# Kernel tuning notes

Hardware: AMD Instinct MI355X
Metric: run time of the kernel (lower is better)

Reference implementation:

```python
import jax, jax.numpy as jnp
import numpy as np

B, NNODES = 65536, 32
D_IN, D_G, D_C, H, D_OUT = 16, 8, 16, 64, 4


def setup_inputs() -> dict:
    key = jax.random.key(0)
    ks = jax.random.split(key, 24)
    N = B * NNODES
    x = jax.random.normal(ks[0], (N, D_IN), jnp.float32)
    other_obs = jax.random.normal(ks[1], (B, D_C), jnp.float32)
    # star graph per batch element with reverse edges: (0->j) and (j->0)
    bs = np.concatenate([np.zeros(NNODES - 1, np.int32), np.arange(1, NNODES, dtype=np.int32)])
    bd = np.concatenate([np.arange(1, NNODES, dtype=np.int32), np.zeros(NNODES - 1, np.int32)])
    offs = (np.arange(B, dtype=np.int32) * NNODES)[:, None]
    src = jnp.asarray((bs[None, :] + offs).reshape(-1))
    dst = jnp.asarray((bd[None, :] + offs).reshape(-1))
    node_seg = jnp.asarray(np.repeat(np.arange(B, dtype=np.int32), NNODES))
    s = 0.1
    p = lambda k, sh: jax.random.normal(k, sh, jnp.float32) * s
    return dict(
        x=x, other_obs=other_obs, src=src, dst=dst, node_seg=node_seg,
        Wp1=p(ks[2], (D_IN, D_G)), bp1=jnp.zeros((D_G,), jnp.float32),
        Ws1=p(ks[3], (D_IN, D_G)), Wn1=p(ks[4], (D_G, D_G)), bc1=jnp.zeros((D_G,), jnp.float32),
        Wp2=p(ks[5], (D_G, D_G)), bp2=jnp.zeros((D_G,), jnp.float32),
        Ws2=p(ks[6], (D_G, D_G)), Wn2=p(ks[7], (D_G, D_G)), bc2=jnp.zeros((D_G,), jnp.float32),
        W1=p(ks[8], (D_C + D_G, H)), bf1=jnp.zeros((H,), jnp.float32),
        W2=p(ks[9], (H, H)), bf2=jnp.zeros((H,), jnp.float32),
        W3=p(ks[10], (H, H)), bf3=jnp.zeros((H,), jnp.float32),
        W4=jax.random.uniform(ks[11], (H, D_OUT), jnp.float32, -0.003, 0.003),
        bf4=jnp.zeros((D_OUT,), jnp.float32),
    )


def _sage_pool(h, src, dst, Wp, bp, Ws, Wn, bc, num_nodes):
    # DGL SAGEConv aggregator_type='pool': relu(fc_pool(h_src)), scatter-max to dst
    m = jax.nn.relu(h @ Wp + bp)[src]              # [E, D_G]
    agg = jax.ops.segment_max(m, dst, num_segments=num_nodes)
    agg = jnp.where(jnp.isfinite(agg), agg, 0.0)   # empty-neighbor nodes -> 0 (DGL default)
    return h @ Ws + agg @ Wn + bc


def reference(x, other_obs, src, dst, node_seg,
              Wp1, bp1, Ws1, Wn1, bc1,
              Wp2, bp2, Ws2, Wn2, bc2,
              W1, bf1, W2, bf2, W3, bf3, W4, bf4):
    N = x.shape[0]
    Bn = other_obs.shape[0]
    n_per = N // Bn
    h = jnp.tanh(_sage_pool(x, src, dst, Wp1, bp1, Ws1, Wn1, bc1, N))  # conv1 activation=tanh
    h = _sage_pool(h, src, dst, Wp2, bp2, Ws2, Wn2, bc2, N)            # conv2, no activation
    pooled = jax.ops.segment_sum(h, node_seg, num_segments=Bn) / n_per  # AvgPooling (fixed n)
    res = jnp.concatenate([pooled, other_obs], axis=1)
    h1 = jax.nn.relu(res @ W1 + bf1)
    h2 = jax.nn.relu(h1 @ W2 + bf2)
    h3 = jax.nn.relu(h2 @ W3 + bf3)
    return jnp.tanh(h3 @ W4 + bf4)
```

## Files before the change

### kernel.cpp

```cpp
#include <hip/hip_runtime.h>


typedef float v2f __attribute__((ext_vector_type(2)));
__device__ __forceinline__ v2f fma2(v2f a, v2f b, v2f c) {
  return __builtin_elementwise_fma(a, b, c);
}
__device__ __forceinline__ v2f ld2(const float* p) { return *(const v2f*)p; }

__device__ __forceinline__ float fast_tanh(float v) {
  v = fminf(fmaxf(v, -10.f), 10.f);
  float e = exp2f(v * 2.8853900817779268f);
  return 1.f - 2.f * __builtin_amdgcn_rcpf(e + 1.f);
}

template<int CTRL, int RMASK>
__device__ __forceinline__ float dpp0(float v) {
  return __int_as_float(__builtin_amdgcn_update_dpp(
      0, __float_as_int(v), CTRL, RMASK, 0xf, true));
}
__device__ __forceinline__ float red_max32(float t) {
  t = fmaxf(t, dpp0<0x111, 0xf>(t));
  t = fmaxf(t, dpp0<0x112, 0xf>(t));
  t = fmaxf(t, dpp0<0x114, 0xf>(t));
  t = fmaxf(t, dpp0<0x118, 0xf>(t));
  t = fmaxf(t, dpp0<0x142, 0xa>(t));
  return t;
}
__device__ __forceinline__ float red_sum32(float t) {
  t += dpp0<0x111, 0xf>(t);
  t += dpp0<0x112, 0xf>(t);
  t += dpp0<0x114, 0xf>(t);
  t += dpp0<0x118, 0xf>(t);
  t += dpp0<0x142, 0xa>(t);
  return t;
}
__device__ __forceinline__ float bcast31(float v) {
  return __int_as_float(__builtin_amdgcn_ds_swizzle(__float_as_int(v), 0x03E0));
}

__global__ __launch_bounds__(256, 4) void conv_kernel(
    const float* __restrict__ x,
    const float* __restrict__ Wp1, const float* __restrict__ bp1,
    const float* __restrict__ Ws1, const float* __restrict__ Wn1,
    const float* __restrict__ bc1,
    const float* __restrict__ Wp2, const float* __restrict__ bp2,
    float* __restrict__ res) {
  const int lane = threadIdx.x & 63;
  const int pair = blockIdx.x * 4 + (threadIdx.x >> 6);
  const int nl = lane & 31, s = lane >> 5;
  const int node = 31 - nl;
  const int b = pair * 2 + s;
  const bool isn0 = (nl == 31);

  const float4* xp = (const float4*)(x + ((size_t)b * 32 + node) * 16);
  float4 a0 = xp[0], a1 = xp[1], a2 = xp[2], a3 = xp[3];
  float xr[16] = {a0.x,a0.y,a0.z,a0.w, a1.x,a1.y,a1.z,a1.w,
                  a2.x,a2.y,a2.z,a2.w, a3.x,a3.y,a3.z,a3.w};

  v2f mv[4], sv[4];
  #pragma unroll
  for (int i = 0; i < 4; i++) { mv[i] = ld2(bp1 + 2*i); sv[i] = ld2(bc1 + 2*i); }
  #pragma unroll
  for (int f = 0; f < 16; f++) {
    v2f xv = {xr[f], xr[f]};
    #pragma unroll
    for (int i = 0; i < 4; i++) {
      mv[i] = fma2(xv, ld2(Wp1 + f*8 + 2*i), mv[i]);
      sv[i] = fma2(xv, ld2(Ws1 + f*8 + 2*i), sv[i]);
    }
  }
  float m[8];
  #pragma unroll
  for (int i = 0; i < 4; i++) {
    m[2*i]   = fmaxf(mv[i].x, 0.f);
    m[2*i+1] = fmaxf(mv[i].y, 0.f);
  }

  float agg[8];
  #pragma unroll
  for (int g = 0; g < 8; g++) {
    float t = isn0 ? 0.f : m[g];
    t = red_max32(t);
    float b0v = bcast31(m[g]);
    agg[g] = isn0 ? t : b0v;
  }
  #pragma unroll
  for (int j = 0; j < 8; j++) {
    v2f av = {agg[j], agg[j]};
    #pragma unroll
    for (int i = 0; i < 4; i++) sv[i] = fma2(av, ld2(Wn1 + j*8 + 2*i), sv[i]);
  }
  float h[8];
  #pragma unroll
  for (int i = 0; i < 4; i++) {
    h[2*i]   = fast_tanh(sv[i].x);
    h[2*i+1] = fast_tanh(sv[i].y);
  }

  v2f m2v[4];
  #pragma unroll
  for (int i = 0; i < 4; i++) m2v[i] = ld2(bp2 + 2*i);
  #pragma unroll
  for (int j = 0; j < 8; j++) {
    v2f hv = {h[j], h[j]};
    #pragma unroll
    for (int i = 0; i < 4; i++) m2v[i] = fma2(hv, ld2(Wp2 + j*8 + 2*i), m2v[i]);
  }
  float m2[8];
  #pragma unroll
  for (int i = 0; i < 4; i++) {
    m2[2*i]   = fmaxf(m2v[i].x, 0.f);
    m2[2*i+1] = fmaxf(m2v[i].y, 0.f);
  }

  float outv[16];
  #pragma unroll
  for (int g = 0; g < 8; g++) outv[g] = red_sum32(h[g]);
  #pragma unroll
  for (int g = 0; g < 8; g++) {
    float t = isn0 ? 0.f : m2[g];
    t = red_max32(t);
    outv[8+g] = fmaf(31.f, m2[g], t);
  }
  if (isn0) {
    float4* rp = (float4*)(res + (size_t)b * 16);
    rp[0] = make_float4(outv[0],  outv[1],  outv[2],  outv[3]);
    rp[1] = make_float4(outv[4],  outv[5],  outv[6],  outv[7]);
    rp[2] = make_float4(outv[8],  outv[9],  outv[10], outv[11]);
    rp[3] = make_float4(outv[12], outv[13], outv[14], outv[15]);
  }
}

#define HSTR 65
__global__ __launch_bounds__(256, 3) void mlp_kernel(
    const float* __restrict__ res, const float* __restrict__ obs,
    const float* __restrict__ Ws2, const float* __restrict__ Wn2,
    const float* __restrict__ bc2,
    const float* __restrict__ W1, const float* __restrict__ bf1,
    const float* __restrict__ W2, const float* __restrict__ bf2,
    const float* __restrict__ W3, const float* __restrict__ bf3,
    const float* __restrict__ W4, const float* __restrict__ bf4,
    float* __restrict__ out) {
  __shared__ float hx[64 * HSTR];
  const int tid  = threadIdx.x;
  const int lane = tid & 63;
  const int p    = __builtin_amdgcn_readfirstlane(tid >> 6);
  const int b    = blockIdx.x * 64 + lane;
  const int ob0  = p * 16;

  const float4* rp = (const float4*)(res + (size_t)b * 16);
  float4 r0 = rp[0], r1 = rp[1], r2 = rp[2], r3 = rp[3];
  const float4* op = (const float4*)(obs + (size_t)b * 16);
  float4 o0 = op[0], o1 = op[1], o2 = op[2], o3 = op[3];
  float rm[8] = {r0.x,r0.y,r0.z,r0.w, r1.x,r1.y,r1.z,r1.w};
  float ag[8] = {r2.x,r2.y,r2.z,r2.w, r3.x,r3.y,r3.z,r3.w};
  float ob[16] = {o0.x,o0.y,o0.z,o0.w, o1.x,o1.y,o1.z,o1.w,
                  o2.x,o2.y,o2.z,o2.w, o3.x,o3.y,o3.z,o3.w};

  v2f pv[4];
  #pragma unroll
  for (int i = 0; i < 4; i++) pv[i] = (v2f){0.f, 0.f};
  #pragma unroll
  for (int j = 0; j < 8; j++) {
    v2f rv = {rm[j], rm[j]}, av = {ag[j], ag[j]};
    #pragma unroll
    for (int i = 0; i < 4; i++) {
      pv[i] = fma2(rv, ld2(Ws2 + j*8 + 2*i), pv[i]);
      pv[i] = fma2(av, ld2(Wn2 + j*8 + 2*i), pv[i]);
    }
  }
  float pooled[8];
  #pragma unroll
  for (int i = 0; i < 4; i++) {
    pooled[2*i]   = fmaf(pv[i].x, 1.f/32.f, bc2[2*i]);
    pooled[2*i+1] = fmaf(pv[i].y, 1.f/32.f, bc2[2*i+1]);
  }

  v2f acc[8];
  #pragma unroll
  for (int i = 0; i < 8; i++) acc[i] = ld2(bf1 + ob0 + 2*i);
  #pragma unroll
  for (int j = 0; j < 8; j++) {
    v2f sj = {pooled[j], pooled[j]};
    #pragma unroll
    for (int i = 0; i < 8; i++) acc[i] = fma2(sj, ld2(W1 + j*64 + ob0 + 2*i), acc[i]);
  }
  #pragma unroll
  for (int j = 0; j < 16; j++) {
    v2f sj = {ob[j], ob[j]};
    #pragma unroll
    for (int i = 0; i < 8; i++) acc[i] = fma2(sj, ld2(W1 + (8+j)*64 + ob0 + 2*i), acc[i]);
  }
  #pragma unroll
  for (int i = 0; i < 8; i++) {
    hx[lane*HSTR + ob0 + 2*i]   = fmaxf(acc[i].x, 0.f);
    hx[lane*HSTR + ob0 + 2*i+1] = fmaxf(acc[i].y, 0.f);
  }
  __syncthreads();
  float h[64];
  #pragma unroll
  for (int k = 0; k < 64; k++) h[k] = hx[lane*HSTR + k];
  __syncthreads();

  #pragma unroll
  for (int i = 0; i < 8; i++) acc[i] = ld2(bf2 + ob0 + 2*i);
  #pragma unroll
  for (int k = 0; k < 64; k++) {
    v2f hk = {h[k], h[k]};
    #pragma unroll
    for (int i = 0; i < 8; i++) acc[i] = fma2(hk, ld2(W2 + k*64 + ob0 + 2*i), acc[i]);
  }
  #pragma unroll
  for (int i = 0; i < 8; i++) {
    hx[lane*HSTR + ob0 + 2*i]   = fmaxf(acc[i].x, 0.f);
    hx[lane*HSTR + ob0 + 2*i+1] = fmaxf(acc[i].y, 0.f);
  }
  __syncthreads();
  #pragma unroll
  for (int k = 0; k < 64; k++) h[k] = hx[lane*HSTR + k];
  __syncthreads();

  #pragma unroll
  for (int i = 0; i < 8; i++) acc[i] = ld2(bf3 + ob0 + 2*i);
  #pragma unroll
  for (int k = 0; k < 64; k++) {
    v2f hk = {h[k], h[k]};
    #pragma unroll
    for (int i = 0; i < 8; i++) acc[i] = fma2(hk, ld2(W3 + k*64 + ob0 + 2*i), acc[i]);
  }
  #pragma unroll
  for (int i = 0; i < 8; i++) {
    hx[lane*HSTR + ob0 + 2*i]   = fmaxf(acc[i].x, 0.f);
    hx[lane*HSTR + ob0 + 2*i+1] = fmaxf(acc[i].y, 0.f);
  }
  __syncthreads();

  if (p == 0) {
    #pragma unroll
    for (int k = 0; k < 64; k++) h[k] = hx[lane*HSTR + k];
    v2f o4a = ld2(bf4), o4b = ld2(bf4 + 2);
    #pragma unroll
    for (int k = 0; k < 64; k++) {
      v2f hk = {h[k], h[k]};
      o4a = fma2(hk, ld2(W4 + k*4),     o4a);
      o4b = fma2(hk, ld2(W4 + k*4 + 2), o4b);
    }
    ((float4*)out)[b] = make_float4(fast_tanh(o4a.x), fast_tanh(o4a.y),
                                    fast_tanh(o4b.x), fast_tanh(o4b.y));
  }
}

extern "C" void kernel_launch(void* const* d_in, const int* in_sizes, int n_in,
                              void* d_out, int out_size, void* d_ws, size_t ws_size,
                              hipStream_t stream) {
  const float* x   = (const float*)d_in[0];
  const float* obs = (const float*)d_in[1];
  const float* Wp1 = (const float*)d_in[5];
  const float* bp1 = (const float*)d_in[6];
  const float* Ws1 = (const float*)d_in[7];
  const float* Wn1 = (const float*)d_in[8];
  const float* bc1 = (const float*)d_in[9];
  const float* Wp2 = (const float*)d_in[10];
  const float* bp2 = (const float*)d_in[11];
  const float* Ws2 = (const float*)d_in[12];
  const float* Wn2 = (const float*)d_in[13];
  const float* bc2 = (const float*)d_in[14];
  const float* W1  = (const float*)d_in[15];
  const float* bf1 = (const float*)d_in[16];
  const float* W2  = (const float*)d_in[17];
  const float* bf2 = (const float*)d_in[18];
  const float* W3  = (const float*)d_in[19];
  const float* bf3 = (const float*)d_in[20];
  const float* W4  = (const float*)d_in[21];
  const float* bf4 = (const float*)d_in[22];
  float* res = (float*)d_ws;
  float* out = (float*)d_out;

  hipLaunchKernelGGL(conv_kernel, dim3(8192), dim3(256), 0, stream,
                     x, Wp1, bp1, Ws1, Wn1, bc1, Wp2, bp2, res);
  hipLaunchKernelGGL(mlp_kernel, dim3(1024), dim3(256), 0, stream,
                     res, obs, Ws2, Wn2, bc2, W1, bf1, W2, bf2, W3, bf3, W4, bf4, out);
}
```

Measured before the change: 283.0 us.

## Process two nodes per lane in conv kernel with 16-lane graph groups

Each lane now handles two nodes of a batch graph, so a graph occupies 16 lanes instead of 32 and the grid is halved. Cross-lane max and sum reductions drop one DPP step, and the two nodes are combined inside the lane before reducing. Weight loads are shared between the two nodes, which cuts reduction and broadcast overhead per node. In exchange each thread holds more registers, which may lower occupancy, and each lane reads 32 contiguous floats per node pair.

New measurement: 285.8 us. About the same (+1.0%).

```diff
diff --git a/kernel.cpp b/kernel.cpp
--- a/kernel.cpp
+++ b/kernel.cpp
@@ -18,24 +18,46 @@
   return __int_as_float(__builtin_amdgcn_update_dpp(
       0, __float_as_int(v), CTRL, RMASK, 0xf, true));
 }
-__device__ __forceinline__ float red_max32(float t) {
+__device__ __forceinline__ float red_max16(float t) {
   t = fmaxf(t, dpp0<0x111, 0xf>(t));
   t = fmaxf(t, dpp0<0x112, 0xf>(t));
   t = fmaxf(t, dpp0<0x114, 0xf>(t));
   t = fmaxf(t, dpp0<0x118, 0xf>(t));
-  t = fmaxf(t, dpp0<0x142, 0xa>(t));
   return t;
 }
-__device__ __forceinline__ float red_sum32(float t) {
+__device__ __forceinline__ float red_sum16(float t) {
   t += dpp0<0x111, 0xf>(t);
   t += dpp0<0x112, 0xf>(t);
   t += dpp0<0x114, 0xf>(t);
   t += dpp0<0x118, 0xf>(t);
-  t += dpp0<0x142, 0xa>(t);
   return t;
 }
-__device__ __forceinline__ float bcast31(float v) {
-  return __int_as_float(__builtin_amdgcn_ds_swizzle(__float_as_int(v), 0x03E0));
+__device__ __forceinline__ float bcast15(float v) {
+  return __int_as_float(__builtin_amdgcn_ds_swizzle(__float_as_int(v), 0x01F0));
+}
+
+__device__ __forceinline__ void conv1_node(
+    const float xr[16],
+    const float* __restrict__ Wp1, const float* __restrict__ bp1,
+    const float* __restrict__ Ws1, const float* __restrict__ bc1,
+    float m[8], v2f sv[4]) {
+  v2f mv[4];
+  #pragma unroll
+  for (int i = 0; i < 4; i++) { mv[i] = ld2(bp1 + 2*i); sv[i] = ld2(bc1 + 2*i); }
+  #pragma unroll
+  for (int f = 0; f < 16; f++) {
+    v2f xv = {xr[f], xr[f]};
+    #pragma unroll
+    for (int i = 0; i < 4; i++) {
+      mv[i] = fma2(xv, ld2(Wp1 + f*8 + 2*i), mv[i]);
+      sv[i] = fma2(xv, ld2(Ws1 + f*8 + 2*i), sv[i]);
+    }
+  }
+  #pragma unroll
+  for (int i = 0; i < 4; i++) {
+    m[2*i]   = fmaxf(mv[i].x, 0.f);
+    m[2*i+1] = fmaxf(mv[i].y, 0.f);
+  }
 }
 
 __global__ __launch_bounds__(256, 4) void conv_kernel(
@@ -45,82 +67,89 @@
     const float* __restrict__ bc1,
     const float* __restrict__ Wp2, const float* __restrict__ bp2,
     float* __restrict__ res) {
-  const int lane = threadIdx.x & 63;
-  const int pair = blockIdx.x * 4 + (threadIdx.x >> 6);
-  const int nl = lane & 31, s = lane >> 5;
-  const int node = 31 - nl;
-  const int b = pair * 2 + s;
-  const bool isn0 = (nl == 31);
-
-  const float4* xp = (const float4*)(x + ((size_t)b * 32 + node) * 16);
-  float4 a0 = xp[0], a1 = xp[1], a2 = xp[2], a3 = xp[3];
-  float xr[16] = {a0.x,a0.y,a0.z,a0.w, a1.x,a1.y,a1.z,a1.w,
-                  a2.x,a2.y,a2.z,a2.w, a3.x,a3.y,a3.z,a3.w};
-
-  v2f mv[4], sv[4];
-  #pragma unroll
-  for (int i = 0; i < 4; i++) { mv[i] = ld2(bp1 + 2*i); sv[i] = ld2(bc1 + 2*i); }
-  #pragma unroll
-  for (int f = 0; f < 16; f++) {
-    v2f xv = {xr[f], xr[f]};
+  const int tid  = threadIdx.x;
+  const int lane = tid & 63;
+  const int l    = lane & 15;
+  const int row  = lane >> 4;
+  const int b    = blockIdx.x * 16 + (tid >> 6) * 4 + row;
+  const int nA   = 30 - 2*l;
+  const bool isn0 = (l == 15);
+
+  const float4* xp = (const float4*)(x + ((size_t)b * 32 + nA) * 16);
+
+  float mA[8], mB[8];
+  v2f svA[4], svB[4];
+  {
+    float4 a0 = xp[0], a1 = xp[1], a2 = xp[2], a3 = xp[3];
+    float xr[16] = {a0.x,a0.y,a0.z,a0.w, a1.x,a1.y,a1.z,a1.w,
+                    a2.x,a2.y,a2.z,a2.w, a3.x,a3.y,a3.z,a3.w};
+    conv1_node(xr, Wp1, bp1, Ws1, bc1, mA, svA);
+  }
+  {
+    float4 a0 = xp[4], a1 = xp[5], a2 = xp[6], a3 = xp[7];
+    float xr[16] = {a0.x,a0.y,a0.z,a0.w, a1.x,a1.y,a1.z,a1.w,
+                    a2.x,a2.y,a2.z,a2.w, a3.x,a3.y,a3.z,a3.w};
+    conv1_node(xr, Wp1, bp1, Ws1, bc1, mB, svB);
+  }
+
+  float aggA[8], aggB[8];
+  #pragma unroll
+  for (int g = 0; g < 8; g++) {
+    float t = isn0 ? mB[g] : fmaxf(mA[g], mB[g]);
+    t = red_max16(t);
+    float b0v = bcast15(mA[g]);
+    aggA[g] = isn0 ? t : b0v;
+    aggB[g] = b0v;
+  }
+  #pragma unroll
+  for (int j = 0; j < 8; j++) {
+    v2f avA = {aggA[j], aggA[j]}, avB = {aggB[j], aggB[j]};
     #pragma unroll
     for (int i = 0; i < 4; i++) {
-      mv[i] = fma2(xv, ld2(Wp1 + f*8 + 2*i), mv[i]);
-      sv[i] = fma2(xv, ld2(Ws1 + f*8 + 2*i), sv[i]);
-    }
-  }
-  float m[8];
+      v2f w = ld2(Wn1 + j*8 + 2*i);
+      svA[i] = fma2(avA, w, svA[i]);
+      svB[i] = fma2(avB, w, svB[i]);
+    }
+  }
+  float hA[8], hB[8];
   #pragma unroll
   for (int i = 0; i < 4; i++) {
-    m[2*i]   = fmaxf(mv[i].x, 0.f);
-    m[2*i+1] = fmaxf(mv[i].y, 0.f);
-  }
-
-  float agg[8];
+    hA[2*i]   = fast_tanh(svA[i].x);
+    hA[2*i+1] = fast_tanh(svA[i].y);
+    hB[2*i]   = fast_tanh(svB[i].x);
+    hB[2*i+1] = fast_tanh(svB[i].y);
+  }
+
+  v2f m2vA[4], m2vB[4];
+  #pragma unroll
+  for (int i = 0; i < 4; i++) { m2vA[i] = ld2(bp2 + 2*i); m2vB[i] = m2vA[i]; }
+  #pragma unroll
+  for (int j = 0; j < 8; j++) {
+    v2f hvA = {hA[j], hA[j]}, hvB = {hB[j], hB[j]};
+    #pragma unroll
+    for (int i = 0; i < 4; i++) {
+      v2f w = ld2(Wp2 + j*8 + 2*i);
+      m2vA[i] = fma2(hvA, w, m2vA[i]);
+      m2vB[i] = fma2(hvB, w, m2vB[i]);
+    }
+  }
+  float m2A[8], m2B[8];
+  #pragma unroll
+  for (int i = 0; i < 4; i++) {
+    m2A[2*i]   = fmaxf(m2vA[i].x, 0.f);
+    m2A[2*i+1] = fmaxf(m2vA[i].y, 0.f);
+    m2B[2*i]   = fmaxf(m2vB[i].x, 0.f);
+    m2B[2*i+1] = fmaxf(m2vB[i].y, 0.f);
+  }
+
+  float outv[16];
+  #pragma unroll
+  for (int g = 0; g < 8; g++) outv[g] = red_sum16(hA[g] + hB[g]);
   #pragma unroll
   for (int g = 0; g < 8; g++) {
-    float t = isn0 ? 0.f : m[g];
-    t = red_max32(t);
-    float b0v = bcast31(m[g]);
-    agg[g] = isn0 ? t : b0v;
-  }
-  #pragma unroll
-  for (int j = 0; j < 8; j++) {
-    v2f av = {agg[j], agg[j]};
-    #pragma unroll
-    for (int i = 0; i < 4; i++) sv[i] = fma2(av, ld2(Wn1 + j*8 + 2*i), sv[i]);
-  }
-  float h[8];
-  #pragma unroll
-  for (int i = 0; i < 4; i++) {
-    h[2*i]   = fast_tanh(sv[i].x);
-    h[2*i+1] = fast_tanh(sv[i].y);
-  }
-
-  v2f m2v[4];
-  #pragma unroll
-  for (int i = 0; i < 4; i++) m2v[i] = ld2(bp2 + 2*i);
-  #pragma unroll
-  for (int j = 0; j < 8; j++) {
-    v2f hv = {h[j], h[j]};
-    #pragma unroll
-    for (int i = 0; i < 4; i++) m2v[i] = fma2(hv, ld2(Wp2 + j*8 + 2*i), m2v[i]);
-  }
-  float m2[8];
-  #pragma unroll
-  for (int i = 0; i < 4; i++) {
-    m2[2*i]   = fmaxf(m2v[i].x, 0.f);
-    m2[2*i+1] = fmaxf(m2v[i].y, 0.f);
-  }
-
-  float outv[16];
-  #pragma unroll
-  for (int g = 0; g < 8; g++) outv[g] = red_sum32(h[g]);
-  #pragma unroll
-  for (int g = 0; g < 8; g++) {
-    float t = isn0 ? 0.f : m2[g];
-    t = red_max32(t);
-    outv[8+g] = fmaf(31.f, m2[g], t);
+    float t = isn0 ? m2B[g] : fmaxf(m2A[g], m2B[g]);
+    t = red_max16(t);
+    outv[8+g] = fmaf(31.f, m2A[g], t);
   }
   if (isn0) {
     float4* rp = (float4*)(res + (size_t)b * 16);
@@ -276,7 +305,7 @@
   float* res = (float*)d_ws;
   float* out = (float*)d_out;
 
-  hipLaunchKernelGGL(conv_kernel, dim3(8192), dim3(256), 0, stream,
+  hipLaunchKernelGGL(conv_kernel, dim3(4096), dim3(256), 0, stream,
                      x, Wp1, bp1, Ws1, Wn1, bc1, Wp2, bp2, res);
   hipLaunchKernelGGL(mlp_kernel, dim3(1024), dim3(256), 0, stream,
                      res, obs, Ws2, Wn2, bc2, W1, bf1, W2, bf2, W3, bf3, W4, bf4, out);
```

## Remap conv kernel to channel-per-lane layout with LDS exchange and batch loop

Applied to the files above, without the earlier changes.

Rewrites the graph-conv kernel so each lane owns one output channel for four nodes (8 channels by 8 node groups per wave), holding weight columns in registers instead of reloading them per FMA. Cross-node max and sum reductions become three-step ds_swizzle butterflies plus small LDS exchanges for the hub node's features and the hidden vectors. Each wave now processes four batch elements in a loop with half the grid. The intent is to cut redundant weight loads and the per-node 8-wide reductions. In exchange it adds LDS traffic, uses strided per-lane x loads that may coalesce poorly, and lowers the occupancy hint.

Result: slower. 354.0 us (+25.1%).

```diff
diff --git a/kernel.cpp b/kernel.cpp
--- a/kernel.cpp
+++ b/kernel.cpp
@@ -13,121 +13,120 @@
   return 1.f - 2.f * __builtin_amdgcn_rcpf(e + 1.f);
 }
 
-template<int CTRL, int RMASK>
-__device__ __forceinline__ float dpp0(float v) {
-  return __int_as_float(__builtin_amdgcn_update_dpp(
-      0, __float_as_int(v), CTRL, RMASK, 0xf, true));
-}
-__device__ __forceinline__ float red_max32(float t) {
-  t = fmaxf(t, dpp0<0x111, 0xf>(t));
-  t = fmaxf(t, dpp0<0x112, 0xf>(t));
-  t = fmaxf(t, dpp0<0x114, 0xf>(t));
-  t = fmaxf(t, dpp0<0x118, 0xf>(t));
-  t = fmaxf(t, dpp0<0x142, 0xa>(t));
+template<int OFF>
+__device__ __forceinline__ float swz(float v) {
+  return __int_as_float(__builtin_amdgcn_ds_swizzle(__float_as_int(v), OFF));
+}
+__device__ __forceinline__ float bflymax8(float t) {
+  t = fmaxf(t, swz<0x041F>(t));
+  t = fmaxf(t, swz<0x081F>(t));
+  t = fmaxf(t, swz<0x101F>(t));
   return t;
 }
-__device__ __forceinline__ float red_sum32(float t) {
-  t += dpp0<0x111, 0xf>(t);
-  t += dpp0<0x112, 0xf>(t);
-  t += dpp0<0x114, 0xf>(t);
-  t += dpp0<0x118, 0xf>(t);
-  t += dpp0<0x142, 0xa>(t);
+__device__ __forceinline__ float bflysum8(float t) {
+  t += swz<0x041F>(t);
+  t += swz<0x081F>(t);
+  t += swz<0x101F>(t);
   return t;
 }
-__device__ __forceinline__ float bcast31(float v) {
-  return __int_as_float(__builtin_amdgcn_ds_swizzle(__float_as_int(v), 0x03E0));
-}
-
-__global__ __launch_bounds__(256, 4) void conv_kernel(
+
+#define NB 4
+#define HPAD 12
+__global__ __launch_bounds__(256, 3) void conv_kernel(
     const float* __restrict__ x,
     const float* __restrict__ Wp1, const float* __restrict__ bp1,
     const float* __restrict__ Ws1, const float* __restrict__ Wn1,
     const float* __restrict__ bc1,
     const float* __restrict__ Wp2, const float* __restrict__ bp2,
     float* __restrict__ res) {
-  const int lane = threadIdx.x & 63;
-  const int pair = blockIdx.x * 4 + (threadIdx.x >> 6);
-  const int nl = lane & 31, s = lane >> 5;
-  const int node = 31 - nl;
-  const int b = pair * 2 + s;
-  const bool isn0 = (nl == 31);
-
-  const float4* xp = (const float4*)(x + ((size_t)b * 32 + node) * 16);
-  float4 a0 = xp[0], a1 = xp[1], a2 = xp[2], a3 = xp[3];
-  float xr[16] = {a0.x,a0.y,a0.z,a0.w, a1.x,a1.y,a1.z,a1.w,
-                  a2.x,a2.y,a2.z,a2.w, a3.x,a3.y,a3.z,a3.w};
-
-  v2f mv[4], sv[4];
-  #pragma unroll
-  for (int i = 0; i < 4; i++) { mv[i] = ld2(bp1 + 2*i); sv[i] = ld2(bc1 + 2*i); }
-  #pragma unroll
-  for (int f = 0; f < 16; f++) {
-    v2f xv = {xr[f], xr[f]};
-    #pragma unroll
-    for (int i = 0; i < 4; i++) {
-      mv[i] = fma2(xv, ld2(Wp1 + f*8 + 2*i), mv[i]);
-      sv[i] = fma2(xv, ld2(Ws1 + f*8 + 2*i), sv[i]);
-    }
-  }
-  float m[8];
-  #pragma unroll
-  for (int i = 0; i < 4; i++) {
-    m[2*i]   = fmaxf(mv[i].x, 0.f);
-    m[2*i+1] = fmaxf(mv[i].y, 0.f);
-  }
-
-  float agg[8];
-  #pragma unroll
-  for (int g = 0; g < 8; g++) {
-    float t = isn0 ? 0.f : m[g];
-    t = red_max32(t);
-    float b0v = bcast31(m[g]);
-    agg[g] = isn0 ? t : b0v;
-  }
-  #pragma unroll
-  for (int j = 0; j < 8; j++) {
-    v2f av = {agg[j], agg[j]};
-    #pragma unroll
-    for (int i = 0; i < 4; i++) sv[i] = fma2(av, ld2(Wn1 + j*8 + 2*i), sv[i]);
-  }
-  float h[8];
-  #pragma unroll
-  for (int i = 0; i < 4; i++) {
-    h[2*i]   = fast_tanh(sv[i].x);
-    h[2*i+1] = fast_tanh(sv[i].y);
-  }
-
-  v2f m2v[4];
-  #pragma unroll
-  for (int i = 0; i < 4; i++) m2v[i] = ld2(bp2 + 2*i);
-  #pragma unroll
-  for (int j = 0; j < 8; j++) {
-    v2f hv = {h[j], h[j]};
-    #pragma unroll
-    for (int i = 0; i < 4; i++) m2v[i] = fma2(hv, ld2(Wp2 + j*8 + 2*i), m2v[i]);
-  }
-  float m2[8];
-  #pragma unroll
-  for (int i = 0; i < 4; i++) {
-    m2[2*i]   = fmaxf(m2v[i].x, 0.f);
-    m2[2*i+1] = fmaxf(m2v[i].y, 0.f);
-  }
-
-  float outv[16];
-  #pragma unroll
-  for (int g = 0; g < 8; g++) outv[g] = red_sum32(h[g]);
-  #pragma unroll
-  for (int g = 0; g < 8; g++) {
-    float t = isn0 ? 0.f : m2[g];
-    t = red_max32(t);
-    outv[8+g] = fmaf(31.f, m2[g], t);
-  }
-  if (isn0) {
-    float4* rp = (float4*)(res + (size_t)b * 16);
-    rp[0] = make_float4(outv[0],  outv[1],  outv[2],  outv[3]);
-    rp[1] = make_float4(outv[4],  outv[5],  outv[6],  outv[7]);
-    rp[2] = make_float4(outv[8],  outv[9],  outv[10], outv[11]);
-    rp[3] = make_float4(outv[12], outv[13], outv[14], outv[15]);
+  __shared__ __align__(16) float lds[4 * 400];
+  const int tid  = threadIdx.x;
+  const int wid  = tid >> 6;
+  const int lane = tid & 63;
+  const int c    = lane >> 3;
+  const int g    = lane & 7;
+  const bool g0  = (g == 0);
+  float* hl  = lds + wid * 400;
+  float* scr = hl + 384;
+
+  float wp1[16], ws1[16], wn1[8], wp2[8];
+  #pragma unroll
+  for (int f = 0; f < 16; f++) { wp1[f] = Wp1[f*8 + c]; ws1[f] = Ws1[f*8 + c]; }
+  #pragma unroll
+  for (int j = 0; j < 8; j++)  { wn1[j] = Wn1[j*8 + c]; wp2[j] = Wp2[j*8 + c]; }
+  const float bp1c = bp1[c], bc1c = bc1[c], bp2c = bp2[c];
+
+  int b = (blockIdx.x * 4 + wid) * NB;
+  #pragma unroll 1
+  for (int it = 0; it < NB; ++it, ++b) {
+    const float4* xb = (const float4*)(x + ((size_t)b * 32 + 4*g) * 16);
+
+    float m[4], sv[4];
+    #pragma unroll
+    for (int s = 0; s < 4; s++) {
+      float4 X0 = xb[4*s+0], X1 = xb[4*s+1], X2 = xb[4*s+2], X3 = xb[4*s+3];
+      float xf[16] = {X0.x,X0.y,X0.z,X0.w, X1.x,X1.y,X1.z,X1.w,
+                      X2.x,X2.y,X2.z,X2.w, X3.x,X3.y,X3.z,X3.w};
+      float mm = bp1c, ss = bc1c;
+      #pragma unroll
+      for (int f = 0; f < 16; f++) {
+        mm = fmaf(xf[f], wp1[f], mm);
+        ss = fmaf(xf[f], ws1[f], ss);
+      }
+      m[s]  = fmaxf(mm, 0.f);
+      sv[s] = ss;
+    }
+
+    float lm = g0 ? fmaxf(fmaxf(m[1], m[2]), m[3])
+                  : fmaxf(fmaxf(m[0], m[1]), fmaxf(m[2], m[3]));
+    lm = bflymax8(lm);
+
+    if (g0) *(v2f*)(scr + 2*c) = (v2f){m[0], lm};
+    float4 q0 = *(const float4*)(scr + 0);
+    float4 q1 = *(const float4*)(scr + 4);
+    float4 q2 = *(const float4*)(scr + 8);
+    float4 q3 = *(const float4*)(scr + 12);
+    float m0v[8] = {q0.x,q0.z, q1.x,q1.z, q2.x,q2.z, q3.x,q3.z};
+    float mlv[8] = {q0.y,q0.w, q1.y,q1.w, q2.y,q2.w, q3.y,q3.w};
+
+    float leafdot = 0.f, zerodot = 0.f;
+    #pragma unroll
+    for (int j = 0; j < 8; j++) {
+      leafdot = fmaf(m0v[j], wn1[j], leafdot);
+      zerodot = fmaf(mlv[j], wn1[j], zerodot);
+    }
+    float h0 = fast_tanh(sv[0] + (g0 ? zerodot : leafdot));
+    float h1 = fast_tanh(sv[1] + leafdot);
+    float h2 = fast_tanh(sv[2] + leafdot);
+    float h3 = fast_tanh(sv[3] + leafdot);
+
+    hl[(4*g+0)*HPAD + c] = h0;
+    hl[(4*g+1)*HPAD + c] = h1;
+    hl[(4*g+2)*HPAD + c] = h2;
+    hl[(4*g+3)*HPAD + c] = h3;
+
+    float m2[4];
+    #pragma unroll
+    for (int s = 0; s < 4; s++) {
+      const float* hn = hl + (4*g+s)*HPAD;
+      float4 ha = *(const float4*)(hn);
+      float4 hb = *(const float4*)(hn + 4);
+      float mm = bp2c;
+      mm = fmaf(ha.x, wp2[0], mm); mm = fmaf(ha.y, wp2[1], mm);
+      mm = fmaf(ha.z, wp2[2], mm); mm = fmaf(ha.w, wp2[3], mm);
+      mm = fmaf(hb.x, wp2[4], mm); mm = fmaf(hb.y, wp2[5], mm);
+      mm = fmaf(hb.z, wp2[6], mm); mm = fmaf(hb.w, wp2[7], mm);
+      m2[s] = fmaxf(mm, 0.f);
+    }
+
+    float sh = bflysum8((h0 + h1) + (h2 + h3));
+    float lm2 = g0 ? fmaxf(fmaxf(m2[1], m2[2]), m2[3])
+                   : fmaxf(fmaxf(m2[0], m2[1]), fmaxf(m2[2], m2[3]));
+    lm2 = bflymax8(lm2);
+    if (g0) {
+      res[(size_t)b*16 + c]     = sh;
+      res[(size_t)b*16 + 8 + c] = fmaf(31.f, m2[0], lm2);
+    }
   }
 }
 
@@ -276,7 +275,7 @@
   float* res = (float*)d_ws;
   float* out = (float*)d_out;
 
-  hipLaunchKernelGGL(conv_kernel, dim3(8192), dim3(256), 0, stream,
+  hipLaunchKernelGGL(conv_kernel, dim3(4096), dim3(256), 0, stream,
                      x, Wp1, bp1, Ws1, Wn1, bc1, Wp2, bp2, res);
   hipLaunchKernelGGL(mlp_kernel, dim3(1024), dim3(256), 0, stream,
                      res, obs, Ws2, Wn2, bc2, W1, bf1, W2, bf2, W3, bf3, W4, bf4, out);
```
